# Kernel optimization log

Measured on AMD Instinct MI355X. Metric: run time of the kernel, lower is better.

## Reference

```python
import jax, jax.numpy as jnp
import numpy as np

B, C_IN, V, C_OUT, K = 4, 64, 50000, 128, 7


def setup_inputs() -> dict:
    key = jax.random.key(0)
    k1, k2, k3, k4 = jax.random.split(key, 4)
    x = jax.random.normal(k1, (B, C_IN, V, 1), dtype=jnp.float32)
    # Gi: per-vertex [self, n1, n2, n3] indices (random neighbors, in-range)
    Gi = jax.random.randint(k2, (B, V, 4), 0, V, dtype=jnp.int64)
    # Conv2d(in, out, kernel=(1,7)) weight collapsed to [out, in, 7]
    W = jax.random.normal(k3, (C_OUT, C_IN, K), dtype=jnp.float32) * 0.05
    b = jax.random.normal(k4, (C_OUT,), dtype=jnp.float32) * 0.05
    return {"x": x, "Gi": Gi, "W": W, "b": b}


def reference(x, Gi, W, b):
    xs = x[..., 0]  # [B, C, V]  (squeeze(-1))
    Bx, C, Vx = xs.shape
    # prepend zero-padding column (index 0 after Gi+1 maps padded -1 entries)
    xp = jnp.concatenate([jnp.zeros((Bx, C, 1), xs.dtype), xs], axis=2)  # [B,C,V+1]
    gi = Gi + 1
    # gather per batch: f[b,c,v,j] = xp[b,c,gi[b,v,j]]
    f = jax.vmap(lambda xb, gb: xb[:, gb])(xp, gi)  # [B, C, V, 4]
    f0, f1, f2, f3 = f[..., 0], f[..., 1], f[..., 2], f[..., 3]
    G = jnp.stack([
        f0,
        f1 + f2 + f3,                                        # symm_oper 1
        f1 * f2 * f3,                                        # symm_oper 2
        f1 * f2 + f1 * f3 + f2 * f3,                         # symm_oper 3
        f1 * f1 + f2 * f2 + f3 * f3,                         # symm_oper 4
        jnp.abs(f1 - f2) + jnp.abs(f1 - f3) + jnp.abs(f2 - f3),  # symm_oper 5
        f1 * f1 * f1 + f2 * f2 * f2 + f3 * f3 * f3,          # symm_oper 6
    ], axis=3)  # [B, C, V, 7]
    # conv2d with kernel (1,7), no padding -> width collapses to 1
    out = jnp.einsum('bcvk,ock->bov', G, W) + b[None, :, None]
    return out[..., None]  # [B, C_out, V, 1]
```

## Files before the change

kernel.cpp:

```cpp
#include <hip/hip_runtime.h>
#include <hip/hip_bf16.h>
#include <cstdint>
#include <cstddef>

#define BB   4
#define CIN  64
#define VV   50000
#define COUT 128
#define NV   32
#define KTOT 448
#define KT   14
#define PITCH 456

typedef __attribute__((ext_vector_type(8))) short short8;
typedef __attribute__((ext_vector_type(4))) float f32x4;

__device__ float          g_xt[(size_t)BB * VV * CIN];
__device__ unsigned short g_wb[KT * 8 * 64 * 8];

__device__ inline unsigned short f2bf(float f) {
    union { __hip_bfloat16 h; unsigned short u; } cv;
    cv.h = __float2bfloat16(f);
    return cv.u;
}

__global__ __launch_bounds__(256) void transpose_k(const float* __restrict__ x) {
    __shared__ float tile[64][65];
    int b    = blockIdx.y;
    int v0   = blockIdx.x * 64;
    int lane = threadIdx.x & 63;
    int row  = threadIdx.x >> 6;
#pragma unroll
    for (int i = 0; i < 16; i++) {
        int c = row + 4 * i;
        int v = v0 + lane;
        float val = 0.f;
        if (v < VV) val = x[((size_t)b * CIN + c) * VV + v];
        tile[c][lane] = val;
    }
    __syncthreads();
#pragma unroll
    for (int i = 0; i < 16; i++) {
        int v = v0 + row + 4 * i;
        if (v < VV) g_xt[((size_t)b * VV + v) * CIN + lane] = tile[lane][row + 4 * i];
    }
}

__global__ __launch_bounds__(256) void pack_wb_k(const float* __restrict__ W) {
    int idx = blockIdx.x * 256 + threadIdx.x;
    if (idx >= KT * 8 * 64) return;
    int lane = idx & 63;
    int mt   = (idx >> 6) & 7;
    int kt   = idx >> 9;
    int m    = mt * 16 + (lane & 15);
    int kb   = kt * 32 + (lane >> 4) * 8;
    union { unsigned short s[8]; short8 v; } u;
#pragma unroll
    for (int j = 0; j < 8; j++) {
        int kk = kb + j;
        int c  = kk & 63;
        int k  = kk >> 6;
        u.s[j] = f2bf(W[((size_t)m * CIN + c) * 7 + k]);
    }
    *(short8*)&g_wb[(size_t)idx * 8] = u.v;
}

__device__ inline void feats(float f0, float f1, float f2, float f3, float* g) {
    g[0] = f0;
    g[1] = f1 + f2 + f3;
    float p12 = f1 * f2, p13 = f1 * f3, p23 = f2 * f3;
    g[2] = p12 * f3;
    g[3] = p12 + p13 + p23;
    g[4] = f1 * f1 + f2 * f2 + f3 * f3;
    g[5] = fabsf(f1 - f2) + fabsf(f1 - f3) + fabsf(f2 - f3);
    g[6] = f1 * f1 * f1 + f2 * f2 * f2 + f3 * f3 * f3;
}

__global__ __launch_bounds__(256) void mesh_k(
        const void* __restrict__ Gi, const float* __restrict__ bias,
        float* __restrict__ out) {
    __shared__ unsigned short Gl[NV * PITCH];

    int b  = blockIdx.y;
    int v0 = blockIdx.x * NV;
    int t  = threadIdx.x;

    const unsigned* gu = (const unsigned*)Gi;
    bool is64 = ((gu[1] | gu[3] | gu[5] | gu[7]) == 0u);

    int lc2 = t & 31;
    int grp = t >> 5;
#pragma unroll
    for (int p = 0; p < 4; ++p) {
        int vv = p * 8 + grp;
        int v  = v0 + vv;
        unsigned* grow = (unsigned*)&Gl[vv * PITCH + lc2 * 2];
        if (v < VV) {
            long long i0, i1, i2, i3;
            size_t gb = ((size_t)b * VV + v) * 4;
            if (is64) {
                const long long* g8 = (const long long*)Gi + gb;
                i0 = g8[0]; i1 = g8[1]; i2 = g8[2]; i3 = g8[3];
            } else {
                const int* g4 = (const int*)Gi + gb;
                i0 = g4[0]; i1 = g4[1]; i2 = g4[2]; i3 = g4[3];
            }
            int j0 = (int)(i0 < 0 ? 0 : (i0 >= VV ? VV - 1 : i0));
            int j1 = (int)(i1 < 0 ? 0 : (i1 >= VV ? VV - 1 : i1));
            int j2 = (int)(i2 < 0 ? 0 : (i2 >= VV ? VV - 1 : i2));
            int j3 = (int)(i3 < 0 ? 0 : (i3 >= VV ? VV - 1 : i3));

            const float* base = g_xt + (size_t)b * VV * CIN + lc2 * 2;
            float2 f0 = *(const float2*)(base + (size_t)j0 * CIN);
            float2 f1 = *(const float2*)(base + (size_t)j1 * CIN);
            float2 f2 = *(const float2*)(base + (size_t)j2 * CIN);
            float2 f3 = *(const float2*)(base + (size_t)j3 * CIN);

            float gx[7], gy[7];
            feats(f0.x, f1.x, f2.x, f3.x, gx);
            feats(f0.y, f1.y, f2.y, f3.y, gy);
#pragma unroll
            for (int k = 0; k < 7; k++)
                grow[k * 32] = (unsigned)f2bf(gx[k]) | ((unsigned)f2bf(gy[k]) << 16);
        } else {
#pragma unroll
            for (int k = 0; k < 7; k++) grow[k * 32] = 0u;
        }
    }
    __syncthreads();

    int w    = t >> 6;
    int lane = t & 63;
    int l15  = lane & 15;
    int q    = lane >> 4;

    f32x4 acc[2][2] = {};

    const short8* wb = (const short8*)g_wb;
    for (int kt = 0; kt < KT; ++kt) {
        short8 a0 = wb[(kt * 8 + 2 * w    ) * 64 + lane];
        short8 a1 = wb[(kt * 8 + 2 * w + 1) * 64 + lane];
        short8 b0 = *(const short8*)&Gl[(l15     ) * PITCH + kt * 32 + q * 8];
        short8 b1 = *(const short8*)&Gl[(l15 + 16) * PITCH + kt * 32 + q * 8];
        acc[0][0] = __builtin_amdgcn_mfma_f32_16x16x32_bf16(a0, b0, acc[0][0], 0, 0, 0);
        acc[0][1] = __builtin_amdgcn_mfma_f32_16x16x32_bf16(a0, b1, acc[0][1], 0, 0, 0);
        acc[1][0] = __builtin_amdgcn_mfma_f32_16x16x32_bf16(a1, b0, acc[1][0], 0, 0, 0);
        acc[1][1] = __builtin_amdgcn_mfma_f32_16x16x32_bf16(a1, b1, acc[1][1], 0, 0, 0);
    }

#pragma unroll
    for (int mt = 0; mt < 2; ++mt) {
        int o = 32 * w + mt * 16 + q * 4;
        float bs[4];
#pragma unroll
        for (int r = 0; r < 4; ++r) bs[r] = bias[o + r];
#pragma unroll
        for (int nt = 0; nt < 2; ++nt) {
            int v = v0 + nt * 16 + l15;
            if (v < VV) {
                float* po = out + ((size_t)b * COUT + o) * VV + v;
#pragma unroll
                for (int r = 0; r < 4; ++r)
                    po[(size_t)r * VV] = acc[mt][nt][r] + bs[r];
            }
        }
    }
}

extern "C" void kernel_launch(void* const* d_in, const int* in_sizes, int n_in,
                              void* d_out, int out_size, void* d_ws, size_t ws_size,
                              hipStream_t stream) {
    const float* x    = (const float*)d_in[0];
    const void*  Gi   = d_in[1];
    const float* W    = (const float*)d_in[2];
    const float* bias = (const float*)d_in[3];
    float* out        = (float*)d_out;

    dim3 gt((VV + 63) / 64, BB);
    transpose_k<<<gt, 256, 0, stream>>>(x);
    pack_wb_k<<<(KT * 8 * 64 + 255) / 256, 256, 0, stream>>>(W);
    dim3 gm((VV + NV - 1) / NV, BB);
    mesh_k<<<gm, 256, 0, stream>>>(Gi, bias, out);
}
```

Baseline: 230.4 us.

## Vectorize transpose, stage gather indices in LDS, batch all gathers before compute

The transpose kernel now uses float4 loads and stores instead of scalar accesses. The mesh kernel loads the neighbor indices cooperatively into shared memory, then issues all 16 gathers per thread up front before computing features, so more memory requests are in flight at once. The MFMA loop is unrolled by 2. Out-of-range vertices now gather row 0 instead of writing zeros, but those columns are masked on store. More live registers may reduce occupancy.

```diff
diff --git a/kernel.cpp b/kernel.cpp
--- a/kernel.cpp
+++ b/kernel.cpp
@@ -26,23 +26,44 @@
 
 __global__ __launch_bounds__(256) void transpose_k(const float* __restrict__ x) {
     __shared__ float tile[64][65];
-    int b    = blockIdx.y;
-    int v0   = blockIdx.x * 64;
-    int lane = threadIdx.x & 63;
-    int row  = threadIdx.x >> 6;
-#pragma unroll
-    for (int i = 0; i < 16; i++) {
-        int c = row + 4 * i;
-        int v = v0 + lane;
-        float val = 0.f;
-        if (v < VV) val = x[((size_t)b * CIN + c) * VV + v];
-        tile[c][lane] = val;
+    int b  = blockIdx.y;
+    int v0 = blockIdx.x * 64;
+    int t  = threadIdx.x;
+    int tv = t & 15;
+    int tc = t >> 4;
+#pragma unroll
+    for (int i = 0; i < 4; i++) {
+        int c = tc + 16 * i;
+        int v = v0 + tv * 4;
+        const float* src = x + ((size_t)b * CIN + c) * VV + v;
+        float4 f;
+        if (v + 3 < VV) {
+            f = *(const float4*)src;
+        } else {
+            f.x = v + 0 < VV ? src[0] : 0.f;
+            f.y = v + 1 < VV ? src[1] : 0.f;
+            f.z = v + 2 < VV ? src[2] : 0.f;
+            f.w = v + 3 < VV ? src[3] : 0.f;
+        }
+        tile[c][tv * 4 + 0] = f.x;
+        tile[c][tv * 4 + 1] = f.y;
+        tile[c][tv * 4 + 2] = f.z;
+        tile[c][tv * 4 + 3] = f.w;
     }
     __syncthreads();
-#pragma unroll
-    for (int i = 0; i < 16; i++) {
-        int v = v0 + row + 4 * i;
-        if (v < VV) g_xt[((size_t)b * VV + v) * CIN + lane] = tile[lane][row + 4 * i];
+    int c4  = t & 15;
+    int tvv = t >> 4;
+#pragma unroll
+    for (int i = 0; i < 4; i++) {
+        int v = v0 + tvv + 16 * i;
+        if (v < VV) {
+            float4 f;
+            f.x = tile[c4 * 4 + 0][tvv + 16 * i];
+            f.y = tile[c4 * 4 + 1][tvv + 16 * i];
+            f.z = tile[c4 * 4 + 2][tvv + 16 * i];
+            f.w = tile[c4 * 4 + 3][tvv + 16 * i];
+            *(float4*)(g_xt + ((size_t)b * VV + v) * CIN + c4 * 4) = f;
+        }
     }
 }
 
@@ -80,6 +101,7 @@
         const void* __restrict__ Gi, const float* __restrict__ bias,
         float* __restrict__ out) {
     __shared__ unsigned short Gl[NV * PITCH];
+    __shared__ int Sidx[NV][4];
 
     int b  = blockIdx.y;
     int v0 = blockIdx.x * NV;
@@ -88,44 +110,45 @@
     const unsigned* gu = (const unsigned*)Gi;
     bool is64 = ((gu[1] | gu[3] | gu[5] | gu[7]) == 0u);
 
+    if (t < NV * 4) {
+        int vv = t >> 2, j = t & 3;
+        int v  = v0 + vv;
+        long long val = 0;
+        if (v < VV) {
+            size_t gb = ((size_t)b * VV + v) * 4 + j;
+            val = is64 ? ((const long long*)Gi)[gb] : (long long)((const int*)Gi)[gb];
+        }
+        Sidx[vv][j] = (int)(val < 0 ? 0 : (val >= VV ? VV - 1 : val));
+    }
+    __syncthreads();
+
     int lc2 = t & 31;
     int grp = t >> 5;
+    int J[4][4];
 #pragma unroll
     for (int p = 0; p < 4; ++p) {
         int vv = p * 8 + grp;
-        int v  = v0 + vv;
+#pragma unroll
+        for (int j = 0; j < 4; ++j) J[p][j] = Sidx[vv][j];
+    }
+    const float* base = g_xt + (size_t)b * VV * CIN + lc2 * 2;
+    float2 F[4][4];
+#pragma unroll
+    for (int p = 0; p < 4; ++p)
+#pragma unroll
+        for (int j = 0; j < 4; ++j)
+            F[p][j] = *(const float2*)(base + (size_t)J[p][j] * CIN);
+
+#pragma unroll
+    for (int p = 0; p < 4; ++p) {
+        int vv = p * 8 + grp;
         unsigned* grow = (unsigned*)&Gl[vv * PITCH + lc2 * 2];
-        if (v < VV) {
-            long long i0, i1, i2, i3;
-            size_t gb = ((size_t)b * VV + v) * 4;
-            if (is64) {
-                const long long* g8 = (const long long*)Gi + gb;
-                i0 = g8[0]; i1 = g8[1]; i2 = g8[2]; i3 = g8[3];
-            } else {
-                const int* g4 = (const int*)Gi + gb;
-                i0 = g4[0]; i1 = g4[1]; i2 = g4[2]; i3 = g4[3];
-            }
-            int j0 = (int)(i0 < 0 ? 0 : (i0 >= VV ? VV - 1 : i0));
-            int j1 = (int)(i1 < 0 ? 0 : (i1 >= VV ? VV - 1 : i1));
-            int j2 = (int)(i2 < 0 ? 0 : (i2 >= VV ? VV - 1 : i2));
-            int j3 = (int)(i3 < 0 ? 0 : (i3 >= VV ? VV - 1 : i3));
-
-            const float* base = g_xt + (size_t)b * VV * CIN + lc2 * 2;
-            float2 f0 = *(const float2*)(base + (size_t)j0 * CIN);
-            float2 f1 = *(const float2*)(base + (size_t)j1 * CIN);
-            float2 f2 = *(const float2*)(base + (size_t)j2 * CIN);
-            float2 f3 = *(const float2*)(base + (size_t)j3 * CIN);
-
-            float gx[7], gy[7];
-            feats(f0.x, f1.x, f2.x, f3.x, gx);
-            feats(f0.y, f1.y, f2.y, f3.y, gy);
-#pragma unroll
-            for (int k = 0; k < 7; k++)
-                grow[k * 32] = (unsigned)f2bf(gx[k]) | ((unsigned)f2bf(gy[k]) << 16);
-        } else {
-#pragma unroll
-            for (int k = 0; k < 7; k++) grow[k * 32] = 0u;
-        }
+        float gx[7], gy[7];
+        feats(F[p][0].x, F[p][1].x, F[p][2].x, F[p][3].x, gx);
+        feats(F[p][0].y, F[p][1].y, F[p][2].y, F[p][3].y, gy);
+#pragma unroll
+        for (int k = 0; k < 7; k++)
+            grow[k * 32] = (unsigned)f2bf(gx[k]) | ((unsigned)f2bf(gy[k]) << 16);
     }
     __syncthreads();
 
@@ -137,6 +160,7 @@
     f32x4 acc[2][2] = {};
 
     const short8* wb = (const short8*)g_wb;
+#pragma unroll 2
     for (int kt = 0; kt < KT; ++kt) {
         short8 a0 = wb[(kt * 8 + 2 * w    ) * 64 + lane];
         short8 a1 = wb[(kt * 8 + 2 * w + 1) * 64 + lane];
```

Measured after the change: 217.7 us. -5.5%, faster.
